# Optimization experiments

Measured on AMD Instinct MI355X. Metric: run time of the kernel, lower is better.

Reference implementation:

```python
import jax, jax.numpy as jnp
import numpy as np

MARGIN = 0.2
LAMBDA_LSE = 6.0
LAMBDA_SOFTMAX = 9.0
EPS = 1e-8


def setup_inputs() -> dict:
    key = jax.random.key(0)
    k1, k2, k3 = jax.random.split(key, 3)
    I, R, W, D = 128, 36, 24, 512
    images = jax.random.normal(k1, (I, R, D), dtype=jnp.float32)
    captions = jax.random.normal(k2, (I, W, D), dtype=jnp.float32)
    # ragged caption lengths in [4, 24]
    cap_lens = 4 + jax.random.randint(k3, (I,), 0, W - 3, dtype=jnp.int32)
    return {"images": images, "captions": captions, "cap_lens": cap_lens}


def _scan_t2i_loss(images, captions, cap_lens):
    # images: [I, R, D]; captions: [C, W, D]; cap_lens: [C]
    C, W, D = captions.shape
    wmask = jnp.arange(W)[None, :] < cap_lens[:, None]          # [C, W] valid-word mask

    # raw attention: bmm(context=images, query^T=caption) -> [C, I, R, W]
    attn = jnp.einsum('ird,cwd->cirw', images, captions)
    # clipped_l2norm: LeakyReLU(0.1) then l2-normalize over word axis;
    # zero padded words so norms match the per-caption sliced computation
    a = jnp.where(attn > 0, attn, 0.1 * attn) * wmask[:, None, None, :]
    a = a / (jnp.sqrt(jnp.sum(a * a, axis=3, keepdims=True)) + EPS)
    # softmax over regions (sourceL) with temperature lambda_softmax
    s = jax.nn.softmax(a * LAMBDA_SOFTMAX, axis=2)              # [C, I, R, W]
    # weighted context per word: [C, I, W, D]
    wei = jnp.einsum('cirw,ird->ciwd', s, images)

    cap = captions[:, None, :, :]                               # [C, 1, W, D]
    num = jnp.sum(cap * wei, axis=-1)                           # [C, I, W]
    den = jnp.clip(jnp.linalg.norm(cap, axis=-1) * jnp.linalg.norm(wei, axis=-1), EPS)
    cos = num / den                                             # [C, I, W]

    # LogSumExp aggregation over valid words
    neg = jnp.finfo(cos.dtype).min
    logits = jnp.where(wmask[:, None, :], cos * LAMBDA_LSE, neg)
    row_sim = jax.nn.logsumexp(logits, axis=-1) / LAMBDA_LSE    # [C, I]
    scores = row_sim.T                                          # [I, C] (image x caption)

    diag = jnp.diag(scores)[:, None]                            # [I, 1]
    cost_s = jnp.clip(MARGIN + scores - diag, 0.0)
    cost_im = jnp.clip(MARGIN + scores - diag.T, 0.0)
    eye = jnp.eye(scores.shape[0], dtype=bool)
    cost_s = jnp.where(eye, 0.0, cost_s)
    cost_im = jnp.where(eye, 0.0, cost_im)
    # max_violation=True: hardest negatives
    cost_s = jnp.max(cost_s, axis=1)
    cost_im = jnp.max(cost_im, axis=0)
    return jnp.sum(cost_s) + jnp.sum(cost_im)


def reference(images, captions, cap_lens):
    return _scan_t2i_loss(images, captions, cap_lens)
```

## Files before the change

kernel.cpp:

```cpp
#include <hip/hip_runtime.h>
#include <math.h>

#define I_N 128
#define C_N 128
#define R_N 36
#define W_N 24
#define D_N 512
#define M_N (I_N * R_N)
#define N_N (C_N * W_N)

typedef __attribute__((ext_vector_type(8))) short bf16x8;
typedef __attribute__((ext_vector_type(4))) float f32x4;
typedef __attribute__((ext_vector_type(8))) unsigned short u16x8;
typedef _Float16 f16x2 __attribute__((ext_vector_type(2)));
typedef __fp16 h16x2 __attribute__((ext_vector_type(2)));

__device__ inline float bf2f(unsigned short u) {
    return __uint_as_float(((unsigned int)u) << 16);
}
__device__ inline unsigned short f2bf(float f) {
    unsigned int u = __float_as_uint(f);
    u = (u + 0x7FFFu + ((u >> 16) & 1u)) >> 16;
    return (unsigned short)u;
}
__device__ inline void gload_lds16(const void* g, void* l) {
    __builtin_amdgcn_global_load_lds(
        (const __attribute__((address_space(1))) void*)g,
        (__attribute__((address_space(3))) void*)l, 16, 0, 0);
}

#if __has_builtin(__builtin_amdgcn_fdot2)
__device__ inline float fdot2f(f16x2 a, f16x2 b, float c) {
    return __builtin_amdgcn_fdot2(__builtin_bit_cast(h16x2, a),
                                  __builtin_bit_cast(h16x2, b), c, false);
}
#else
__device__ inline float fdot2f(f16x2 a, f16x2 b, float c) {
    return c + (float)a[0] * (float)b[0] + (float)a[1] * (float)b[1];
}
#endif

#if __has_builtin(__builtin_amdgcn_cvt_pkrtz)
__device__ inline f16x2 pkf16(float a, float b) {
    return __builtin_bit_cast(f16x2, __builtin_amdgcn_cvt_pkrtz(a, b));
}
#else
__device__ inline f16x2 pkf16(float a, float b) {
    f16x2 v; v[0] = (_Float16)a; v[1] = (_Float16)b; return v;
}
#endif

__global__ __launch_bounds__(256) void prologue_kernel(const float* __restrict__ images,
                                                       const float* __restrict__ captions,
                                                       unsigned short* __restrict__ imgbf,
                                                       unsigned short* __restrict__ capbf,
                                                       float* __restrict__ capn,
                                                       unsigned int* __restrict__ G2) {
    __shared__ float tile[R_N][68];
    __shared__ float gshf[R_N][R_N];
    const int bid = blockIdx.x;
    const int tid = threadIdx.x;
    if (bid < I_N) {
        const int i = bid;
        const float* img = images + (size_t)i * R_N * D_N;
        const int t1 = (tid / 12) * 3;
        const int t2 = (tid % 12) * 3;
        const bool active = tid < 144;
        float acc[3][3] = {{0.f,0.f,0.f},{0.f,0.f,0.f},{0.f,0.f,0.f}};
        for (int k0 = 0; k0 < D_N; k0 += 64) {
            for (int idx = tid; idx < R_N * 16; idx += 256) {
                int r = idx / 16, k4 = idx % 16;
                float4 v = *(const float4*)(img + (size_t)r * D_N + k0 + k4 * 4);
                *(float4*)&tile[r][k4 * 4] = v;
            }
            __syncthreads();
            if (active) {
                #pragma unroll
                for (int k = 0; k < 64; k += 4) {
                    float4 a0 = *(const float4*)&tile[t1 + 0][k];
                    float4 a1 = *(const float4*)&tile[t1 + 1][k];
                    float4 a2 = *(const float4*)&tile[t1 + 2][k];
                    float4 b0 = *(const float4*)&tile[t2 + 0][k];
                    float4 b1 = *(const float4*)&tile[t2 + 1][k];
                    float4 b2 = *(const float4*)&tile[t2 + 2][k];
                    acc[0][0] += a0.x*b0.x + a0.y*b0.y + a0.z*b0.z + a0.w*b0.w;
                    acc[0][1] += a0.x*b1.x + a0.y*b1.y + a0.z*b1.z + a0.w*b1.w;
                    acc[0][2] += a0.x*b2.x + a0.y*b2.y + a0.z*b2.z + a0.w*b2.w;
                    acc[1][0] += a1.x*b0.x + a1.y*b0.y + a1.z*b0.z + a1.w*b0.w;
                    acc[1][1] += a1.x*b1.x + a1.y*b1.y + a1.z*b1.z + a1.w*b1.w;
                    acc[1][2] += a1.x*b2.x + a1.y*b2.y + a1.z*b2.z + a1.w*b2.w;
                    acc[2][0] += a2.x*b0.x + a2.y*b0.y + a2.z*b0.z + a2.w*b0.w;
                    acc[2][1] += a2.x*b1.x + a2.y*b1.y + a2.z*b1.z + a2.w*b1.w;
                    acc[2][2] += a2.x*b2.x + a2.y*b2.y + a2.z*b2.z + a2.w*b2.w;
                }
            }
            __syncthreads();
        }
        if (active) {
            #pragma unroll
            for (int a = 0; a < 3; ++a)
                #pragma unroll
                for (int b = 0; b < 3; ++b)
                    gshf[t1 + a][t2 + b] = acc[a][b];
        }
        __syncthreads();
        unsigned int* gp = G2 + (size_t)i * (R_N * 20);
        for (int idx = tid; idx < R_N * 20; idx += 256) {
            int r = idx / 20, p = idx % 20;
            f16x2 v;
            if (p < 18) v = pkf16(gshf[r][2 * p], gshf[r][2 * p + 1]);
            else { v[0] = (_Float16)0.f; v[1] = (_Float16)0.f; }
            gp[idx] = __builtin_bit_cast(unsigned int, v);
        }
    } else if (bid < I_N + 1152) {
        int idx = (bid - I_N) * 256 + tid;
        float4 v0 = *(const float4*)(images + (size_t)idx * 8);
        float4 v1 = *(const float4*)(images + (size_t)idx * 8 + 4);
        u16x8 o;
        o[0] = f2bf(v0.x); o[1] = f2bf(v0.y); o[2] = f2bf(v0.z); o[3] = f2bf(v0.w);
        o[4] = f2bf(v1.x); o[5] = f2bf(v1.y); o[6] = f2bf(v1.z); o[7] = f2bf(v1.w);
        *(u16x8*)(imgbf + (size_t)idx * 8) = o;
    } else {
        const int crow = (bid - I_N - 1152) * 4 + (tid >> 6);
        const int lane = tid & 63;
        const float* p = captions + (size_t)crow * D_N + lane * 8;
        float4 v0 = *(const float4*)p;
        float4 v1 = *(const float4*)(p + 4);
        u16x8 o;
        o[0] = f2bf(v0.x); o[1] = f2bf(v0.y); o[2] = f2bf(v0.z); o[3] = f2bf(v0.w);
        o[4] = f2bf(v1.x); o[5] = f2bf(v1.y); o[6] = f2bf(v1.z); o[7] = f2bf(v1.w);
        *(u16x8*)(capbf + (size_t)crow * D_N + lane * 8) = o;
        float s = v0.x*v0.x + v0.y*v0.y + v0.z*v0.z + v0.w*v0.w
                + v1.x*v1.x + v1.y*v1.y + v1.z*v1.z + v1.w*v1.w;
        #pragma unroll
        for (int off = 32; off > 0; off >>= 1) s += __shfl_down(s, off);
        if (lane == 0) capn[crow] = sqrtf(s);
    }
}

#define BM 128
#define BN 128
#define BK 32
#define KT (D_N / BK)
#define GX (M_N / BM)
#define GY (N_N / BN)

__global__ __launch_bounds__(256, 4) void attn_gemm_kernel(const unsigned short* __restrict__ A,
                                                           const unsigned short* __restrict__ B,
                                                           unsigned short* __restrict__ attn) {
    __shared__ unsigned short AsBuf[2][BM * BK];
    __shared__ unsigned short BsBuf[2][BN * BK];
    const int flat = blockIdx.x;
    const int nf = (flat & 7) * (GX * GY / 8) + (flat >> 3);
    const int m0 = (nf / GY) * BM;
    const int n0 = (nf % GY) * BN;
    const int tid = threadIdx.x;
    const int lane = tid & 63;
    const int wid = tid >> 6;
    const int wr = wid >> 1, wc = wid & 1;
    const int fr = lane & 15;
    const int fk = lane >> 4;

    const int srow = tid >> 2;
    const int sslot = (tid & 3) ^ (srow & 3) ^ ((srow >> 2) & 3);
    const unsigned short* srcA = A + (size_t)(m0 + srow) * D_N + sslot * 8;
    const unsigned short* srcB = B + (size_t)(n0 + srow) * D_N + sslot * 8;
    const int ldst = tid * 16;
    const int rswz = (fk ^ (fr & 3) ^ ((fr >> 2) & 3)) << 4;

    f32x4 acc[4][4];
    #pragma unroll
    for (int m = 0; m < 4; ++m)
        #pragma unroll
        for (int n = 0; n < 4; ++n) acc[m][n] = (f32x4){0.f, 0.f, 0.f, 0.f};

    #define STAGE(t, buf)                                                              \
        {                                                                              \
            const unsigned short* _a = srcA + (t) * BK;                                \
            const unsigned short* _b = srcB + (t) * BK;                                \
            gload_lds16(_a, (char*)AsBuf[buf] + ldst);                                 \
            gload_lds16(_a + (size_t)64 * D_N, (char*)AsBuf[buf] + 4096 + ldst);       \
            gload_lds16(_b, (char*)BsBuf[buf] + ldst);                                 \
            gload_lds16(_b + (size_t)64 * D_N, (char*)BsBuf[buf] + 4096 + ldst);       \
        }

    STAGE(0, 0)
    STAGE(1, 1)
    asm volatile("s_waitcnt vmcnt(4)" ::: "memory");
    __builtin_amdgcn_sched_barrier(0);
    __builtin_amdgcn_s_barrier();
    __builtin_amdgcn_sched_barrier(0);

    #pragma unroll
    for (int t = 0; t < KT; ++t) {
        const int cur = t & 1;
        const unsigned short* As = AsBuf[cur];
        const unsigned short* Bs = BsBuf[cur];
        bf16x8 af[4], bfr[4];
        #pragma unroll
        for (int m = 0; m < 4; ++m) {
            int rl = wr * 64 + m * 16 + fr;
            af[m] = *(const bf16x8*)((const char*)As + rl * 64 + rswz);
        }
        #pragma unroll
        for (int n = 0; n < 4; ++n) {
            int rl = wc * 64 + n * 16 + fr;
            bfr[n] = *(const bf16x8*)((const char*)Bs + rl * 64 + rswz);
        }
        #pragma unroll
        for (int m = 0; m < 4; ++m)
            #pragma unroll
            for (int n = 0; n < 4; ++n)
                acc[m][n] = __builtin_amdgcn_mfma_f32_16x16x32_bf16(af[m], bfr[n], acc[m][n], 0, 0, 0);
        __builtin_amdgcn_sched_barrier(0);
        __builtin_amdgcn_s_barrier();
        __builtin_amdgcn_sched_barrier(0);
        if (t + 2 < KT) STAGE(t + 2, cur)
        if (t + 1 < KT) {
            if (t + 2 < KT) {
                asm volatile("s_waitcnt vmcnt(4)" ::: "memory");
            } else {
                asm volatile("s_waitcnt vmcnt(0)" ::: "memory");
            }
            __builtin_amdgcn_sched_barrier(0);
            __builtin_amdgcn_s_barrier();
            __builtin_amdgcn_sched_barrier(0);
        }
    }
    #undef STAGE

    #pragma unroll
    for (int m = 0; m < 4; ++m) {
        #pragma unroll
        for (int n = 0; n < 4; ++n) {
            #pragma unroll
            for (int j = 0; j < 4; ++j) {
                int row = m0 + wr * 64 + m * 16 + fk * 4 + j;
                int col = n0 + wc * 64 + n * 16 + fr;
                int i = row / R_N, r = row - i * R_N;
                int c = col / W_N, w = col - c * W_N;
                attn[(((size_t)i * C_N + c) * R_N + r) * W_N + w] = f2bf(acc[m][n][j]);
            }
        }
    }
}

#define CG 8
#define SCL9 12.98425537f

__global__ __launch_bounds__(192) void score_kernel(const unsigned short* __restrict__ attn,
                                                    const unsigned int* __restrict__ G2,
                                                    const float* __restrict__ capn,
                                                    const int* __restrict__ cap_lens,
                                                    float* __restrict__ scores) {
    __shared__ unsigned short stage[CG * R_N * W_N];
    __shared__ __align__(16) unsigned int gsh2[R_N * 20];
    __shared__ float scl_sh[CG * R_N];
    __shared__ float red[CG][W_N];
    __shared__ int len_sh[CG];
    const int i = blockIdx.x;
    const int c0 = blockIdx.y * CG;
    const int tid = threadIdx.x;

    if (tid < CG) len_sh[tid] = cap_lens[c0 + tid];
    const unsigned short* at = attn + ((size_t)i * C_N + c0) * R_N * W_N;
    for (int ch = tid; ch < CG * R_N * W_N / 8; ch += 192)
        *(u16x8*)&stage[ch * 8] = *(const u16x8*)(at + ch * 8);
    const unsigned int* gp = G2 + (size_t)i * (R_N * 20);
    if (tid < 180) ((uint4*)gsh2)[tid] = ((const uint4*)gp)[tid];
    __syncthreads();

    for (int row = tid; row < CG * R_N; row += 192) {
        int cl = row / R_N;
        int len = len_sh[cl];
        const unsigned short* rp = &stage[row * W_N];
        u16x8 p0 = *(const u16x8*)&rp[0];
        u16x8 p1 = *(const u16x8*)&rp[8];
        u16x8 p2 = *(const u16x8*)&rp[16];
        float ss = 0.f;
        #pragma unroll
        for (int q = 0; q < 8; ++q) {
            float x0 = bf2f(p0[q]); x0 = x0 > 0.f ? x0 : 0.1f * x0; x0 = (q      < len) ? x0 : 0.f;
            float x1 = bf2f(p1[q]); x1 = x1 > 0.f ? x1 : 0.1f * x1; x1 = (q + 8  < len) ? x1 : 0.f;
            float x2 = bf2f(p2[q]); x2 = x2 > 0.f ? x2 : 0.1f * x2; x2 = (q + 16 < len) ? x2 : 0.f;
            ss += x0 * x0 + x1 * x1 + x2 * x2;
        }
        scl_sh[row] = SCL9 / (sqrtf(ss) + 1e-8f);
    }
    __syncthreads();

    {
        const int cl = tid / W_N, w = tid - cl * W_N;
        const int len = len_sh[cl];
        const bool valid = w < len;
        const unsigned short* sb = &stage[cl * R_N * W_N];
        const float* sclp = &scl_sh[cl * R_N];
        f16x2 ep[18];
        float Z = 0.f, nu = 0.f;
        float e_prev = 0.f;
        #pragma unroll
        for (int r = 0; r < R_N; ++r) {
            float raw = bf2f(sb[r * W_N + w]);
            float x = raw > 0.f ? raw : 0.1f * raw;
            float l = valid ? x * sclp[r] : 0.f;
            float e = exp2f(l);
            Z += e;
            nu += e * raw;
            if (r & 1) ep[r >> 1] = pkf16(e_prev, e);
            else e_prev = e;
        }
        float wn = 0.f;
        #pragma unroll
        for (int r2 = 0; r2 < R_N; ++r2) {
            const unsigned int* grow = &gsh2[r2 * 20];
            uint4 q0 = *(const uint4*)(grow + 0);
            uint4 q1 = *(const uint4*)(grow + 4);
            uint4 q2 = *(const uint4*)(grow + 8);
            uint4 q3 = *(const uint4*)(grow + 12);
            uint2 q4 = *(const uint2*)(grow + 16);
            unsigned int gq[18] = {q0.x, q0.y, q0.z, q0.w, q1.x, q1.y, q1.z, q1.w,
                                   q2.x, q2.y, q2.z, q2.w, q3.x, q3.y, q3.z, q3.w,
                                   q4.x, q4.y};
            float t0 = 0.f, t1 = 0.f;
            #pragma unroll
            for (int p = 0; p < 18; ++p) {
                f16x2 g = __builtin_bit_cast(f16x2, gq[p]);
                if (p & 1) t1 = fdot2f(g, ep[p], t1);
                else       t0 = fdot2f(g, ep[p], t0);
            }
            wn += (t0 + t1) * (float)ep[r2 >> 1][r2 & 1];
        }
        float iZ = 1.f / Z;
        float cn = capn[(c0 + cl) * W_N + w];
        float den = fmaxf(cn * sqrtf(fmaxf(wn, 0.f)) * iZ, 1e-8f);
        red[cl][w] = valid ? (nu * iZ) / den * 6.0f : -3.4e38f;
    }
    __syncthreads();
    if (tid < CG) {
        float se = 0.f;
        #pragma unroll
        for (int w = 0; w < W_N; ++w) se += __expf(red[tid][w] - 6.0f);
        scores[(size_t)(c0 + tid) * I_N + i] = (__logf(se) + 6.0f) / 6.0f;
    }
}

__global__ __launch_bounds__(128) void final_kernel(const float* __restrict__ scores,
                                                    float* __restrict__ out) {
    __shared__ float diag[C_N];
    __shared__ float red[C_N];
    const int t = threadIdx.x;
    diag[t] = scores[t * C_N + t];
    __syncthreads();
    const float di = diag[t];
    float cs = 0.f, cim = 0.f;
    for (int k = 0; k < C_N; ++k) {
        if (k == t) continue;
        float vs = 0.2f + scores[k * C_N + t] - di;
        float vi = 0.2f + scores[t * C_N + k] - di;
        cs = fmaxf(cs, vs);
        cim = fmaxf(cim, vi);
    }
    red[t] = cs + cim;
    __syncthreads();
    #pragma unroll
    for (int off = 64; off > 0; off >>= 1) {
        if (t < off) red[t] += red[t + off];
        __syncthreads();
    }
    if (t == 0) out[0] = red[0];
}

extern "C" void kernel_launch(void* const* d_in, const int* in_sizes, int n_in,
                              void* d_out, int out_size, void* d_ws, size_t ws_size,
                              hipStream_t stream) {
    (void)in_sizes; (void)n_in; (void)out_size; (void)ws_size;
    const float* images = (const float*)d_in[0];
    const float* captions = (const float*)d_in[1];
    const int* cap_lens = (const int*)d_in[2];
    float* out = (float*)d_out;

    char* wsb = (char*)d_ws;
    size_t off = 0;
    auto alloc = [&](size_t bytes) -> char* {
        char* p = wsb + off;
        off += (bytes + 255) & ~(size_t)255;
        return p;
    };
    unsigned short* imgbf = (unsigned short*)alloc((size_t)M_N * D_N * 2);
    unsigned short* capbf = (unsigned short*)alloc((size_t)N_N * D_N * 2);
    unsigned int* G2 = (unsigned int*)alloc((size_t)I_N * R_N * 20 * 4);
    float* capn = (float*)alloc((size_t)C_N * W_N * 4);
    float* scores = (float*)alloc((size_t)C_N * I_N * 4);
    unsigned short* attn = (unsigned short*)alloc((size_t)I_N * C_N * R_N * W_N * 2);

    prologue_kernel<<<2048, 256, 0, stream>>>(images, captions, imgbf, capbf, capn, G2);
    attn_gemm_kernel<<<GX * GY, 256, 0, stream>>>(imgbf, capbf, attn);
    score_kernel<<<dim3(I_N, C_N / CG), 192, 0, stream>>>(attn, G2, capn, cap_lens, scores);
    final_kernel<<<1, 128, 0, stream>>>(scores, out);
}
```

Baseline: 113.4 us.

## Compact valid caption words so the attention GEMM skips padded columns

An extra prologue block builds a prefix-sum over caption lengths, plus tables mapping compacted column indices to caption rows and (caption, word) pairs. The attention GEMM now gathers B rows through this table, returns early for column tiles beyond the valid count, and scatters outputs only for valid columns. This removes the matmul and store work for padded words, roughly 40% of columns on average. The cost is indirect loads, a serial single-thread prefix sum, and padded attn entries left unwritten, which the score kernel must ignore through its masking.

```diff
diff --git a/kernel.cpp b/kernel.cpp
--- a/kernel.cpp
+++ b/kernel.cpp
@@ -52,14 +52,42 @@
 
 __global__ __launch_bounds__(256) void prologue_kernel(const float* __restrict__ images,
                                                        const float* __restrict__ captions,
+                                                       const int* __restrict__ cap_lens,
                                                        unsigned short* __restrict__ imgbf,
                                                        unsigned short* __restrict__ capbf,
                                                        float* __restrict__ capn,
-                                                       unsigned int* __restrict__ G2) {
+                                                       unsigned int* __restrict__ G2,
+                                                       int* __restrict__ NVp,
+                                                       int* __restrict__ crow_tab,
+                                                       int* __restrict__ cw_tab) {
     __shared__ float tile[R_N][68];
     __shared__ float gshf[R_N][R_N];
     const int bid = blockIdx.x;
     const int tid = threadIdx.x;
+    if (bid == 2048) {
+        __shared__ int S_sh[C_N + 1];
+        if (tid == 0) {
+            int s = 0;
+            for (int c = 0; c < C_N; ++c) { S_sh[c] = s; s += cap_lens[c]; }
+            S_sh[C_N] = s;
+            NVp[0] = s;
+        }
+        __syncthreads();
+        const int NV = S_sh[C_N];
+        if (tid < C_N) {
+            int base = S_sh[tid];
+            int len = cap_lens[tid];
+            for (int w = 0; w < len; ++w) {
+                crow_tab[base + w] = tid * W_N + w;
+                cw_tab[base + w] = (tid << 5) | w;
+            }
+        }
+        for (int idx = NV + tid; idx < N_N; idx += 256) {
+            crow_tab[idx] = 0;
+            cw_tab[idx] = 0;
+        }
+        return;
+    }
     if (bid < I_N) {
         const int i = bid;
         const float* img = images + (size_t)i * R_N * D_N;
@@ -147,6 +175,9 @@
 
 __global__ __launch_bounds__(256, 4) void attn_gemm_kernel(const unsigned short* __restrict__ A,
                                                            const unsigned short* __restrict__ B,
+                                                           const int* __restrict__ NVp,
+                                                           const int* __restrict__ crow_tab,
+                                                           const int* __restrict__ cw_tab,
                                                            unsigned short* __restrict__ attn) {
     __shared__ unsigned short AsBuf[2][BM * BK];
     __shared__ unsigned short BsBuf[2][BN * BK];
@@ -154,6 +185,8 @@
     const int nf = (flat & 7) * (GX * GY / 8) + (flat >> 3);
     const int m0 = (nf / GY) * BM;
     const int n0 = (nf % GY) * BN;
+    const int NV = NVp[0];
+    if (n0 >= NV) return;
     const int tid = threadIdx.x;
     const int lane = tid & 63;
     const int wid = tid >> 6;
@@ -164,7 +197,10 @@
     const int srow = tid >> 2;
     const int sslot = (tid & 3) ^ (srow & 3) ^ ((srow >> 2) & 3);
     const unsigned short* srcA = A + (size_t)(m0 + srow) * D_N + sslot * 8;
-    const unsigned short* srcB = B + (size_t)(n0 + srow) * D_N + sslot * 8;
+    const int crow0 = crow_tab[n0 + srow];
+    const int crow1 = crow_tab[n0 + srow + 64];
+    const unsigned short* srcB0 = B + (size_t)crow0 * D_N + sslot * 8;
+    const unsigned short* srcB1 = B + (size_t)crow1 * D_N + sslot * 8;
     const int ldst = tid * 16;
     const int rswz = (fk ^ (fr & 3) ^ ((fr >> 2) & 3)) << 4;
 
@@ -176,12 +212,11 @@
 
     #define STAGE(t, buf)                                                              \
         {                                                                              \
-            const unsigned short* _a = srcA + (t) * BK;                                \
-            const unsigned short* _b = srcB + (t) * BK;                                \
-            gload_lds16(_a, (char*)AsBuf[buf] + ldst);                                 \
-            gload_lds16(_a + (size_t)64 * D_N, (char*)AsBuf[buf] + 4096 + ldst);       \
-            gload_lds16(_b, (char*)BsBuf[buf] + ldst);                                 \
-            gload_lds16(_b + (size_t)64 * D_N, (char*)BsBuf[buf] + 4096 + ldst);       \
+            gload_lds16(srcA + (t) * BK, (char*)AsBuf[buf] + ldst);                    \
+            gload_lds16(srcA + (size_t)64 * D_N + (t) * BK,                            \
+                        (char*)AsBuf[buf] + 4096 + ldst);                              \
+            gload_lds16(srcB0 + (t) * BK, (char*)BsBuf[buf] + ldst);                   \
+            gload_lds16(srcB1 + (t) * BK, (char*)BsBuf[buf] + 4096 + ldst);            \
         }
 
     STAGE(0, 0)
@@ -230,16 +265,19 @@
     #undef STAGE
 
     #pragma unroll
-    for (int m = 0; m < 4; ++m) {
-        #pragma unroll
-        for (int n = 0; n < 4; ++n) {
+    for (int n = 0; n < 4; ++n) {
+        int ccol = n0 + wc * 64 + n * 16 + fr;
+        if (ccol < NV) {
+            int cw = cw_tab[ccol];
+            int c = cw >> 5, w = cw & 31;
             #pragma unroll
-            for (int j = 0; j < 4; ++j) {
-                int row = m0 + wr * 64 + m * 16 + fk * 4 + j;
-                int col = n0 + wc * 64 + n * 16 + fr;
-                int i = row / R_N, r = row - i * R_N;
-                int c = col / W_N, w = col - c * W_N;
-                attn[(((size_t)i * C_N + c) * R_N + r) * W_N + w] = f2bf(acc[m][n][j]);
+            for (int m = 0; m < 4; ++m) {
+                #pragma unroll
+                for (int j = 0; j < 4; ++j) {
+                    int row = m0 + wr * 64 + m * 16 + fk * 4 + j;
+                    int i = row / R_N, r = row - i * R_N;
+                    attn[(((size_t)i * C_N + c) * R_N + r) * W_N + w] = f2bf(acc[m][n][j]);
+                }
             }
         }
     }
@@ -391,10 +429,15 @@
     unsigned int* G2 = (unsigned int*)alloc((size_t)I_N * R_N * 20 * 4);
     float* capn = (float*)alloc((size_t)C_N * W_N * 4);
     float* scores = (float*)alloc((size_t)C_N * I_N * 4);
+    int* NVp = (int*)alloc(256);
+    int* crow_tab = (int*)alloc((size_t)N_N * 4);
+    int* cw_tab = (int*)alloc((size_t)N_N * 4);
     unsigned short* attn = (unsigned short*)alloc((size_t)I_N * C_N * R_N * W_N * 2);
 
-    prologue_kernel<<<2048, 256, 0, stream>>>(images, captions, imgbf, capbf, capn, G2);
-    attn_gemm_kernel<<<GX * GY, 256, 0, stream>>>(imgbf, capbf, attn);
+    prologue_kernel<<<2049, 256, 0, stream>>>(images, captions, cap_lens,
+                                              imgbf, capbf, capn, G2,
+                                              NVp, crow_tab, cw_tab);
+    attn_gemm_kernel<<<GX * GY, 256, 0, stream>>>(imgbf, capbf, NVp, crow_tab, cw_tab, attn);
     score_kernel<<<dim3(I_N, C_N / CG), 192, 0, stream>>>(attn, G2, capn, cap_lens, scores);
     final_kernel<<<1, 128, 0, stream>>>(scores, out);
 }
```

Measured after the change: 111.9 us, median of 3. Within noise of the previous version (-1.3%).
